# Optimization experiments

Measured on AMD Instinct MI355X. Metric: run time of the kernel, lower is better.

Reference implementation:

```python
import jax, jax.numpy as jnp
import numpy as np

B = 64            # batch size (number of segments)
PTS = 4096        # points per segment
N = B * PTS       # total points
OBS = 128
ACT = 5
HID = 256
LAT = 64
CTX = 128
TEMP = 1.0
LOG2PIE = float(np.log(2.0 * np.pi * np.e))


def _p(key, shape, scale=0.02):
    return (scale * jax.random.normal(key, shape)).astype(jnp.float32)


def setup_inputs() -> dict:
    key = jax.random.key(0)
    ks = jax.random.split(key, 20)
    inp = {
        'obs': jax.random.normal(ks[0], (N, OBS), dtype=jnp.float32),
        'action': jax.random.normal(ks[1], (B, ACT), dtype=jnp.float32),
        'coh_scalar': jax.random.normal(ks[2], (B, 1), dtype=jnp.float32),
        'coh_spatial': jax.random.normal(ks[3], (N,), dtype=jnp.float32),
        'h_prev': jnp.zeros((B, HID), jnp.float32),
        'z_prev': jnp.zeros((B, LAT), jnp.float32),
        'batch': jnp.repeat(jnp.arange(B, dtype=jnp.int64), PTS),
    }
    xin = LAT + ACT + 1  # GRU input: [z_prev, action, coh_scalar]
    inp['W_ih'] = _p(ks[4], (3 * HID, xin)); inp['b_ih'] = jnp.zeros((3 * HID,), jnp.float32)
    inp['W_hh'] = _p(ks[5], (3 * HID, HID)); inp['b_hh'] = jnp.zeros((3 * HID,), jnp.float32)
    inp['W_prior'] = _p(ks[6], (2 * LAT, HID)); inp['b_prior'] = jnp.zeros((2 * LAT,), jnp.float32)
    inp['W_post'] = _p(ks[7], (2 * LAT, HID + OBS)); inp['b_post'] = jnp.zeros((2 * LAT,), jnp.float32)
    inp['W_ae1'] = _p(ks[8], (256, OBS)); inp['b_ae1'] = jnp.zeros((256,), jnp.float32)
    inp['W_ae2'] = _p(ks[9], (OBS, 256)); inp['b_ae2'] = jnp.zeros((OBS,), jnp.float32)
    inp['W_c1'] = _p(ks[10], (512, HID + LAT + OBS)); inp['b_c1'] = jnp.zeros((512,), jnp.float32)
    inp['W_c2'] = _p(ks[11], (CTX, 512)); inp['b_c2'] = jnp.zeros((CTX,), jnp.float32)
    return inp


def _forward(obs, action, coh_scalar, coh_spatial, h_prev, z_prev, batch,
             W_ih, b_ih, W_hh, b_hh, W_prior, b_prior, W_post, b_post,
             W_ae1, b_ae1, W_ae2, b_ae2, W_c1, b_c1, W_c2, b_c2):
    # --- segment mean of obs (the hot scatter-reduce) ---
    counts = jax.ops.segment_sum(jnp.ones((N,), obs.dtype), batch, num_segments=B)
    obs_sum = jax.ops.segment_sum(obs, batch, num_segments=B)            # (B, OBS)
    obs_agg = obs_sum / jnp.maximum(counts, 1.0)[:, None]

    # --- RSSM: GRU cell over [z_prev, action, coh_scalar] ---
    x = jnp.concatenate([z_prev, action, coh_scalar], axis=-1)           # (B, LAT+ACT+1)
    gi = x @ W_ih.T + b_ih
    gh = h_prev @ W_hh.T + b_hh
    gi_r, gi_z, gi_n = jnp.split(gi, 3, axis=-1)
    gh_r, gh_z, gh_n = jnp.split(gh, 3, axis=-1)
    r = jax.nn.sigmoid(gi_r + gh_r)
    u = jax.nn.sigmoid(gi_z + gh_z)
    n = jnp.tanh(gi_n + r * gh_n)
    h = (1.0 - u) * n + u * h_prev                                       # (B, HID)

    prior = h @ W_prior.T + b_prior
    mu_p, logvar_p = jnp.split(prior, 2, axis=-1)
    post = jnp.concatenate([h, obs_agg], axis=-1) @ W_post.T + b_post
    mu_q, logvar_q = jnp.split(post, 2, axis=-1)
    z = mu_q                                                             # deterministic baseline (B, LAT)

    # --- priority: entropy-based uncertainty, per-segment softmax ---
    uncertainty = 0.5 * jnp.sum(logvar_q + LOG2PIE, axis=-1)             # (B,)
    priority = coh_spatial * uncertainty[batch]                          # (N,)
    s = priority / TEMP
    m = jax.ops.segment_max(s, batch, num_segments=B)
    e = jnp.exp(s - m[batch])
    denom = jax.ops.segment_sum(e, batch, num_segments=B)
    priority_norm = e / jnp.maximum(denom, 1e-12)[batch]                 # (N,)

    # --- attended aggregation (second scatter-reduce) ---
    obs_attended = jax.ops.segment_sum(obs * priority_norm[:, None], batch, num_segments=B)  # (B, OBS)
    obs_enc = jax.nn.relu(obs_attended @ W_ae1.T + b_ae1) @ W_ae2.T + b_ae2                  # (B, OBS)

    ctx_in = jnp.concatenate([h, z, obs_enc], axis=-1)                   # (B, HID+LAT+OBS)
    context = jax.nn.relu(ctx_in @ W_c1.T + b_c1) @ W_c2.T + b_c2        # (B, CTX)
    return h, z, context, priority, priority_norm, uncertainty


def reference(obs, action, coh_scalar, coh_spatial, h_prev, z_prev, batch,
              W_ih, b_ih, W_hh, b_hh, W_prior, b_prior, W_post, b_post,
              W_ae1, b_ae1, W_ae2, b_ae2, W_c1, b_c1, W_c2, b_c2):
    return _forward(obs, action, coh_scalar, coh_spatial, h_prev, z_prev, batch,
                    W_ih, b_ih, W_hh, b_hh, W_prior, b_prior, W_post, b_post,
                    W_ae1, b_ae1, W_ae2, b_ae2, W_c1, b_c1, W_c2, b_c2)
```

## Files before the change

kernel.cpp:

```cpp
#include <hip/hip_runtime.h>
#include <math.h>

#define BB   64
#define PTS  4096
#define NTOT (BB * PTS)
#define OBS  128
#define ACT  5
#define HID  256
#define LAT  64
#define CTX  128
#define LOG2PIE 2.8378770664093453f

#define OFF_H   0
#define OFF_Z   (BB * HID)
#define OFF_CTX (OFF_Z + BB * LAT)
#define OFF_PRI (OFF_CTX + BB * CTX)
#define OFF_PN  (OFF_PRI + NTOT)
#define OFF_UNC (OFF_PN + NTOT)

#define CHUNKS 32
#define RPC    (PTS / CHUNKS)

__device__ __forceinline__ float wsum(float v) {
    #pragma unroll
    for (int off = 32; off > 0; off >>= 1) v += __shfl_xor(v, off, 64);
    return v;
}
__device__ __forceinline__ float wmax(float v) {
    #pragma unroll
    for (int off = 32; off > 0; off >>= 1) v = fmaxf(v, __shfl_xor(v, off, 64));
    return v;
}
__device__ __forceinline__ float sigmoidf_(float x) { return 1.f / (1.f + expf(-x)); }

__global__ __launch_bounds__(256) void phase1_kernel(
        const float* __restrict__ obs, float* __restrict__ part,
        const float* __restrict__ action, const float* __restrict__ coh_scalar,
        const float* __restrict__ h_prev, const float* __restrict__ z_prev,
        const float* __restrict__ W_ih, const float* __restrict__ b_ih,
        const float* __restrict__ W_hh, const float* __restrict__ b_hh,
        float* __restrict__ out) {
    __shared__ float4 lds[256];
    int t = threadIdx.x;
    if (blockIdx.x < BB * CHUNKS) {
        int blk = blockIdx.x;
        int b = blk >> 5, chunk = blk & 31;
        int c4 = t & 31, rg = t >> 5;
        const float4* obs4 = (const float4*)obs;
        size_t row0 = (size_t)b * PTS + (size_t)chunk * RPC;
        float4 acc = make_float4(0.f, 0.f, 0.f, 0.f);
        #pragma unroll
        for (int i = 0; i < RPC / 8; ++i) {
            float4 v = obs4[(row0 + rg + 8 * i) * (OBS / 4) + c4];
            acc.x += v.x; acc.y += v.y; acc.z += v.z; acc.w += v.w;
        }
        lds[t] = acc;
        __syncthreads();
        if (t < 32) {
            float4 s = lds[t];
            #pragma unroll
            for (int k = 1; k < 8; ++k) {
                float4 v = lds[t + 32 * k];
                s.x += v.x; s.y += v.y; s.z += v.z; s.w += v.w;
            }
            ((float4*)part)[(size_t)blk * 32 + t] = s;
        }
    } else {
        int wid = (blockIdx.x - BB * CHUNKS) * 4 + (t >> 6);
        int lane = t & 63;
        int b = wid >> 8, j = wid & 255;

        float x0 = z_prev[b * LAT + lane];
        float x1 = 0.f;
        if (lane < ACT) x1 = action[b * ACT + lane];
        else if (lane == ACT) x1 = coh_scalar[b];
        float hp0 = h_prev[b * HID + lane];
        float hp1 = h_prev[b * HID + lane + 64];
        float hp2 = h_prev[b * HID + lane + 128];
        float hp3 = h_prev[b * HID + lane + 192];

        const float* wir = W_ih + (size_t)j * 70;
        const float* wiz = W_ih + (size_t)(HID + j) * 70;
        const float* win = W_ih + (size_t)(2 * HID + j) * 70;
        const float* whr = W_hh + (size_t)j * HID;
        const float* whz = W_hh + (size_t)(HID + j) * HID;
        const float* whn = W_hh + (size_t)(2 * HID + j) * HID;

        float sr = wir[lane] * x0;
        float sz = wiz[lane] * x0;
        float sn = win[lane] * x0;
        if (lane < 6) {
            sr = fmaf(wir[lane + 64], x1, sr);
            sz = fmaf(wiz[lane + 64], x1, sz);
            sn = fmaf(win[lane + 64], x1, sn);
        }
        sr = fmaf(whr[lane], hp0, sr); sr = fmaf(whr[lane + 64], hp1, sr);
        sr = fmaf(whr[lane + 128], hp2, sr); sr = fmaf(whr[lane + 192], hp3, sr);
        sz = fmaf(whz[lane], hp0, sz); sz = fmaf(whz[lane + 64], hp1, sz);
        sz = fmaf(whz[lane + 128], hp2, sz); sz = fmaf(whz[lane + 192], hp3, sz);
        float sh = whn[lane] * hp0;
        sh = fmaf(whn[lane + 64], hp1, sh);
        sh = fmaf(whn[lane + 128], hp2, sh);
        sh = fmaf(whn[lane + 192], hp3, sh);

        sr = wsum(sr); sz = wsum(sz); sn = wsum(sn); sh = wsum(sh);
        if (lane == 0) {
            float r = sigmoidf_(sr + b_ih[j] + b_hh[j]);
            float u = sigmoidf_(sz + b_ih[HID + j] + b_hh[HID + j]);
            float n = tanhf(sn + b_ih[2 * HID + j] + r * (sh + b_hh[2 * HID + j]));
            float h = (1.f - u) * n + u * h_prev[b * HID + j];
            out[OFF_H + b * HID + j] = h;
        }
    }
}

__global__ __launch_bounds__(1024) void post_softmax_kernel(
        const float* __restrict__ part,
        const float* __restrict__ W_post, const float* __restrict__ b_post,
        const float* __restrict__ coh_spatial, float* __restrict__ out) {
    int b = blockIdx.x, t = threadIdx.x;
    int w = t >> 6, lane = t & 63;
    __shared__ __align__(16) float sv[4096];
    __shared__ float hs[256];
    __shared__ float aggs[128];
    __shared__ float lvs[64];
    __shared__ float red[16];
    __shared__ float uS;

    {
        float4* r4 = (float4*)sv;
        int c4 = t & 31, cg = t >> 5;
        const float4* ap4 = (const float4*)part;
        r4[t] = ap4[((size_t)(b * CHUNKS + cg)) * 32 + c4];
    }
    if (t < 256) hs[t] = out[OFF_H + b * HID + t];
    __syncthreads();
    {
        float4* r4 = (float4*)sv;
        #pragma unroll
        for (int s = 16; s > 0; s >>= 1) {
            if ((t >> 5) < s) {
                float4 v = r4[t + 32 * s];
                r4[t].x += v.x; r4[t].y += v.y; r4[t].z += v.z; r4[t].w += v.w;
            }
            __syncthreads();
        }
        if (t < 32) {
            float4 v = r4[t];
            const float sc = 1.0f / PTS;
            aggs[4 * t]     = v.x * sc; aggs[4 * t + 1] = v.y * sc;
            aggs[4 * t + 2] = v.z * sc; aggs[4 * t + 3] = v.w * sc;
        }
    }
    __syncthreads();

    {
        float x0 = hs[lane], x1 = hs[lane + 64], x2 = hs[lane + 128], x3 = hs[lane + 192];
        float x4 = aggs[lane], x5 = aggs[lane + 64];
        #pragma unroll
        for (int g = 0; g < 2; ++g) {
            int r0 = w * 8 + g * 4;
            const float* w0 = W_post + (size_t)r0 * 384;
            const float* w1 = w0 + 384;
            const float* w2 = w0 + 768;
            const float* w3 = w0 + 1152;
            float a0 = w0[lane] * x0, a1 = w1[lane] * x0, a2 = w2[lane] * x0, a3 = w3[lane] * x0;
            a0 = fmaf(w0[lane + 64],  x1, a0); a1 = fmaf(w1[lane + 64],  x1, a1);
            a2 = fmaf(w2[lane + 64],  x1, a2); a3 = fmaf(w3[lane + 64],  x1, a3);
            a0 = fmaf(w0[lane + 128], x2, a0); a1 = fmaf(w1[lane + 128], x2, a1);
            a2 = fmaf(w2[lane + 128], x2, a2); a3 = fmaf(w3[lane + 128], x2, a3);
            a0 = fmaf(w0[lane + 192], x3, a0); a1 = fmaf(w1[lane + 192], x3, a1);
            a2 = fmaf(w2[lane + 192], x3, a2); a3 = fmaf(w3[lane + 192], x3, a3);
            a0 = fmaf(w0[lane + 256], x4, a0); a1 = fmaf(w1[lane + 256], x4, a1);
            a2 = fmaf(w2[lane + 256], x4, a2); a3 = fmaf(w3[lane + 256], x4, a3);
            a0 = fmaf(w0[lane + 320], x5, a0); a1 = fmaf(w1[lane + 320], x5, a1);
            a2 = fmaf(w2[lane + 320], x5, a2); a3 = fmaf(w3[lane + 320], x5, a3);
            a0 = wsum(a0); a1 = wsum(a1); a2 = wsum(a2); a3 = wsum(a3);
            if (lane == 0) {
                a0 += b_post[r0];     a1 += b_post[r0 + 1];
                a2 += b_post[r0 + 2]; a3 += b_post[r0 + 3];
                if (r0 < LAT) {
                    float* dst = out + OFF_Z + b * LAT + r0;
                    dst[0] = a0; dst[1] = a1; dst[2] = a2; dst[3] = a3;
                } else {
                    float* dst = lvs + (r0 - LAT);
                    dst[0] = a0; dst[1] = a1; dst[2] = a2; dst[3] = a3;
                }
            }
        }
    }
    __syncthreads();

    if (w == 0) {
        float v = lvs[lane];
        v = wsum(v);
        if (lane == 0) {
            float u = 0.5f * v + 32.0f * LOG2PIE;
            uS = u;
            out[OFF_UNC + b] = u;
        }
    }
    __syncthreads();
    float u = uS;

    int base = b * PTS;
    float lmax = -INFINITY;
    #pragma unroll
    for (int i = t; i < PTS; i += 1024) {
        float s = coh_spatial[base + i] * u;
        sv[i] = s;
        out[OFF_PRI + base + i] = s;
        lmax = fmaxf(lmax, s);
    }
    lmax = wmax(lmax);
    if (lane == 0) red[w] = lmax;
    __syncthreads();
    float m = red[0];
    #pragma unroll
    for (int k = 1; k < 16; ++k) m = fmaxf(m, red[k]);
    __syncthreads();
    float lsum = 0.f;
    #pragma unroll
    for (int i = t; i < PTS; i += 1024) {
        float e = expf(sv[i] - m);
        sv[i] = e;
        lsum += e;
    }
    lsum = wsum(lsum);
    if (lane == 0) red[w] = lsum;
    __syncthreads();
    float d = 0.f;
    #pragma unroll
    for (int k = 0; k < 16; ++k) d += red[k];
    float inv = 1.f / fmaxf(d, 1e-12f);
    #pragma unroll
    for (int i = t; i < PTS; i += 1024) {
        out[OFF_PN + base + i] = sv[i] * inv;
    }
}

__global__ __launch_bounds__(256) void attn_part_kernel(
        const float* __restrict__ obs, const float* __restrict__ pn,
        float* __restrict__ att_part) {
    int blk = blockIdx.x;
    int b = blk >> 5, chunk = blk & 31;
    int t = threadIdx.x, c4 = t & 31, rg = t >> 5;
    const float4* obs4 = (const float4*)obs;
    size_t row0 = (size_t)b * PTS + (size_t)chunk * RPC;
    float4 acc = make_float4(0.f, 0.f, 0.f, 0.f);
    #pragma unroll
    for (int i = 0; i < RPC / 8; ++i) {
        size_t r = row0 + rg + 8 * i;
        float wgt = pn[r];
        float4 v = obs4[r * (OBS / 4) + c4];
        acc.x = fmaf(v.x, wgt, acc.x);
        acc.y = fmaf(v.y, wgt, acc.y);
        acc.z = fmaf(v.z, wgt, acc.z);
        acc.w = fmaf(v.w, wgt, acc.w);
    }
    __shared__ float4 lds[256];
    lds[t] = acc;
    __syncthreads();
    if (t < 32) {
        float4 s = lds[t];
        #pragma unroll
        for (int k = 1; k < 8; ++k) {
            float4 v = lds[t + 32 * k];
            s.x += v.x; s.y += v.y; s.z += v.z; s.w += v.w;
        }
        ((float4*)att_part)[(size_t)blk * 32 + t] = s;
    }
}

__global__ __launch_bounds__(1024) void head_kernel(
        const float* __restrict__ att_part,
        const float* __restrict__ W_ae1, const float* __restrict__ b_ae1,
        const float* __restrict__ W_ae2, const float* __restrict__ b_ae2,
        const float* __restrict__ W_c1,  const float* __restrict__ b_c1,
        const float* __restrict__ W_c2,  const float* __restrict__ b_c2,
        float* __restrict__ out) {
    int b = blockIdx.x, t = threadIdx.x;
    int w = t >> 6, lane = t & 63;
    __shared__ float4 red4[1024];
    __shared__ float att[128];
    __shared__ float h1[256];
    __shared__ float ctxin[448];
    __shared__ float c1v[512];

    {
        int c4 = t & 31, chunk = t >> 5;
        const float4* ap4 = (const float4*)att_part;
        red4[t] = ap4[((size_t)(b * CHUNKS + chunk)) * 32 + c4];
    }
    if (t < 256) ctxin[t] = out[OFF_H + b * HID + t];
    else if (t < 320) ctxin[t] = out[OFF_Z + b * LAT + (t - 256)];
    __syncthreads();
    #pragma unroll
    for (int s = 16; s > 0; s >>= 1) {
        if ((t >> 5) < s) {
            float4 v = red4[t + 32 * s];
            red4[t].x += v.x; red4[t].y += v.y; red4[t].z += v.z; red4[t].w += v.w;
        }
        __syncthreads();
    }
    if (t < 32) {
        float4 v = red4[t];
        att[4 * t] = v.x; att[4 * t + 1] = v.y; att[4 * t + 2] = v.z; att[4 * t + 3] = v.w;
    }
    __syncthreads();

    {
        float x0 = att[lane], x1 = att[lane + 64];
        #pragma unroll
        for (int g = 0; g < 4; ++g) {
            int r0 = w * 16 + g * 4;
            const float* w0 = W_ae1 + (size_t)(r0 + 0) * OBS;
            const float* w1 = W_ae1 + (size_t)(r0 + 1) * OBS;
            const float* w2 = W_ae1 + (size_t)(r0 + 2) * OBS;
            const float* w3 = W_ae1 + (size_t)(r0 + 3) * OBS;
            float a0 = fmaf(w0[lane + 64], x1, w0[lane] * x0);
            float a1 = fmaf(w1[lane + 64], x1, w1[lane] * x0);
            float a2 = fmaf(w2[lane + 64], x1, w2[lane] * x0);
            float a3 = fmaf(w3[lane + 64], x1, w3[lane] * x0);
            a0 = wsum(a0); a1 = wsum(a1); a2 = wsum(a2); a3 = wsum(a3);
            if (lane == 0) {
                h1[r0]     = fmaxf(a0 + b_ae1[r0],     0.f);
                h1[r0 + 1] = fmaxf(a1 + b_ae1[r0 + 1], 0.f);
                h1[r0 + 2] = fmaxf(a2 + b_ae1[r0 + 2], 0.f);
                h1[r0 + 3] = fmaxf(a3 + b_ae1[r0 + 3], 0.f);
            }
        }
    }
    __syncthreads();

    {
        float x0 = h1[lane], x1 = h1[lane + 64], x2 = h1[lane + 128], x3 = h1[lane + 192];
        #pragma unroll
        for (int g = 0; g < 2; ++g) {
            int r0 = w * 8 + g * 4;
            const float* w0 = W_ae2 + (size_t)(r0 + 0) * 256;
            const float* w1 = W_ae2 + (size_t)(r0 + 1) * 256;
            const float* w2 = W_ae2 + (size_t)(r0 + 2) * 256;
            const float* w3 = W_ae2 + (size_t)(r0 + 3) * 256;
            float a0 = w0[lane] * x0, a1 = w1[lane] * x0, a2 = w2[lane] * x0, a3 = w3[lane] * x0;
            a0 = fmaf(w0[lane + 64], x1, a0);  a1 = fmaf(w1[lane + 64], x1, a1);
            a2 = fmaf(w2[lane + 64], x1, a2);  a3 = fmaf(w3[lane + 64], x1, a3);
            a0 = fmaf(w0[lane + 128], x2, a0); a1 = fmaf(w1[lane + 128], x2, a1);
            a2 = fmaf(w2[lane + 128], x2, a2); a3 = fmaf(w3[lane + 128], x2, a3);
            a0 = fmaf(w0[lane + 192], x3, a0); a1 = fmaf(w1[lane + 192], x3, a1);
            a2 = fmaf(w2[lane + 192], x3, a2); a3 = fmaf(w3[lane + 192], x3, a3);
            a0 = wsum(a0); a1 = wsum(a1); a2 = wsum(a2); a3 = wsum(a3);
            if (lane == 0) {
                ctxin[320 + r0]     = a0 + b_ae2[r0];
                ctxin[320 + r0 + 1] = a1 + b_ae2[r0 + 1];
                ctxin[320 + r0 + 2] = a2 + b_ae2[r0 + 2];
                ctxin[320 + r0 + 3] = a3 + b_ae2[r0 + 3];
            }
        }
    }
    __syncthreads();

    {
        float x0 = ctxin[lane],       x1 = ctxin[lane + 64],  x2 = ctxin[lane + 128];
        float x3 = ctxin[lane + 192], x4 = ctxin[lane + 256], x5 = ctxin[lane + 320];
        float x6 = ctxin[lane + 384];
        #pragma unroll
        for (int g = 0; g < 8; ++g) {
            int r0 = w * 32 + g * 4;
            const float* w0 = W_c1 + (size_t)(r0 + 0) * 448;
            const float* w1 = W_c1 + (size_t)(r0 + 1) * 448;
            const float* w2 = W_c1 + (size_t)(r0 + 2) * 448;
            const float* w3 = W_c1 + (size_t)(r0 + 3) * 448;
            float a0 = w0[lane] * x0, a1 = w1[lane] * x0, a2 = w2[lane] * x0, a3 = w3[lane] * x0;
            a0 = fmaf(w0[lane + 64], x1, a0);  a1 = fmaf(w1[lane + 64], x1, a1);
            a2 = fmaf(w2[lane + 64], x1, a2);  a3 = fmaf(w3[lane + 64], x1, a3);
            a0 = fmaf(w0[lane + 128], x2, a0); a1 = fmaf(w1[lane + 128], x2, a1);
            a2 = fmaf(w2[lane + 128], x2, a2); a3 = fmaf(w3[lane + 128], x2, a3);
            a0 = fmaf(w0[lane + 192], x3, a0); a1 = fmaf(w1[lane + 192], x3, a1);
            a2 = fmaf(w2[lane + 192], x3, a2); a3 = fmaf(w3[lane + 192], x3, a3);
            a0 = fmaf(w0[lane + 256], x4, a0); a1 = fmaf(w1[lane + 256], x4, a1);
            a2 = fmaf(w2[lane + 256], x4, a2); a3 = fmaf(w3[lane + 256], x4, a3);
            a0 = fmaf(w0[lane + 320], x5, a0); a1 = fmaf(w1[lane + 320], x5, a1);
            a2 = fmaf(w2[lane + 320], x5, a2); a3 = fmaf(w3[lane + 320], x5, a3);
            a0 = fmaf(w0[lane + 384], x6, a0); a1 = fmaf(w1[lane + 384], x6, a1);
            a2 = fmaf(w2[lane + 384], x6, a2); a3 = fmaf(w3[lane + 384], x6, a3);
            a0 = wsum(a0); a1 = wsum(a1); a2 = wsum(a2); a3 = wsum(a3);
            if (lane == 0) {
                c1v[r0]     = fmaxf(a0 + b_c1[r0],     0.f);
                c1v[r0 + 1] = fmaxf(a1 + b_c1[r0 + 1], 0.f);
                c1v[r0 + 2] = fmaxf(a2 + b_c1[r0 + 2], 0.f);
                c1v[r0 + 3] = fmaxf(a3 + b_c1[r0 + 3], 0.f);
            }
        }
    }
    __syncthreads();

    {
        float x0 = c1v[lane],       x1 = c1v[lane + 64],  x2 = c1v[lane + 128], x3 = c1v[lane + 192];
        float x4 = c1v[lane + 256], x5 = c1v[lane + 320], x6 = c1v[lane + 384], x7 = c1v[lane + 448];
        #pragma unroll
        for (int g = 0; g < 2; ++g) {
            int r0 = w * 8 + g * 4;
            const float* w0 = W_c2 + (size_t)(r0 + 0) * 512;
            const float* w1 = W_c2 + (size_t)(r0 + 1) * 512;
            const float* w2 = W_c2 + (size_t)(r0 + 2) * 512;
            const float* w3 = W_c2 + (size_t)(r0 + 3) * 512;
            float a0 = w0[lane] * x0, a1 = w1[lane] * x0, a2 = w2[lane] * x0, a3 = w3[lane] * x0;
            a0 = fmaf(w0[lane + 64], x1, a0);  a1 = fmaf(w1[lane + 64], x1, a1);
            a2 = fmaf(w2[lane + 64], x1, a2);  a3 = fmaf(w3[lane + 64], x1, a3);
            a0 = fmaf(w0[lane + 128], x2, a0); a1 = fmaf(w1[lane + 128], x2, a1);
            a2 = fmaf(w2[lane + 128], x2, a2); a3 = fmaf(w3[lane + 128], x2, a3);
            a0 = fmaf(w0[lane + 192], x3, a0); a1 = fmaf(w1[lane + 192], x3, a1);
            a2 = fmaf(w2[lane + 192], x3, a2); a3 = fmaf(w3[lane + 192], x3, a3);
            a0 = fmaf(w0[lane + 256], x4, a0); a1 = fmaf(w1[lane + 256], x4, a1);
            a2 = fmaf(w2[lane + 256], x4, a2); a3 = fmaf(w3[lane + 256], x4, a3);
            a0 = fmaf(w0[lane + 320], x5, a0); a1 = fmaf(w1[lane + 320], x5, a1);
            a2 = fmaf(w2[lane + 320], x5, a2); a3 = fmaf(w3[lane + 320], x5, a3);
            a0 = fmaf(w0[lane + 384], x6, a0); a1 = fmaf(w1[lane + 384], x6, a1);
            a2 = fmaf(w2[lane + 384], x6, a2); a3 = fmaf(w3[lane + 384], x6, a3);
            a0 = fmaf(w0[lane + 448], x7, a0); a1 = fmaf(w1[lane + 448], x7, a1);
            a2 = fmaf(w2[lane + 448], x7, a2); a3 = fmaf(w3[lane + 448], x7, a3);
            a0 = wsum(a0); a1 = wsum(a1); a2 = wsum(a2); a3 = wsum(a3);
            if (lane == 0) {
                float* dst = out + OFF_CTX + b * CTX;
                dst[r0]     = a0 + b_c2[r0];
                dst[r0 + 1] = a1 + b_c2[r0 + 1];
                dst[r0 + 2] = a2 + b_c2[r0 + 2];
                dst[r0 + 3] = a3 + b_c2[r0 + 3];
            }
        }
    }
}

extern "C" void kernel_launch(void* const* d_in, const int* in_sizes, int n_in,
                              void* d_out, int out_size, void* d_ws, size_t ws_size,
                              hipStream_t stream) {
    const float* obs         = (const float*)d_in[0];
    const float* action      = (const float*)d_in[1];
    const float* coh_scalar  = (const float*)d_in[2];
    const float* coh_spatial = (const float*)d_in[3];
    const float* h_prev      = (const float*)d_in[4];
    const float* z_prev      = (const float*)d_in[5];
    const float* W_ih   = (const float*)d_in[7];
    const float* b_ih   = (const float*)d_in[8];
    const float* W_hh   = (const float*)d_in[9];
    const float* b_hh   = (const float*)d_in[10];
    const float* W_post = (const float*)d_in[13];
    const float* b_post = (const float*)d_in[14];
    const float* W_ae1  = (const float*)d_in[15];
    const float* b_ae1  = (const float*)d_in[16];
    const float* W_ae2  = (const float*)d_in[17];
    const float* b_ae2  = (const float*)d_in[18];
    const float* W_c1   = (const float*)d_in[19];
    const float* b_c1   = (const float*)d_in[20];
    const float* W_c2   = (const float*)d_in[21];
    const float* b_c2   = (const float*)d_in[22];

    float* out = (float*)d_out;
    float* part     = (float*)d_ws;
    float* att_part = part + BB * CHUNKS * OBS;

    phase1_kernel<<<BB * CHUNKS + BB * HID / 4, 256, 0, stream>>>(
        obs, part, action, coh_scalar, h_prev, z_prev, W_ih, b_ih, W_hh, b_hh, out);
    post_softmax_kernel<<<BB, 1024, 0, stream>>>(part, W_post, b_post, coh_spatial, out);
    attn_part_kernel<<<BB * CHUNKS, 256, 0, stream>>>(obs, out + OFF_PN, att_part);
    head_kernel<<<BB, 1024, 0, stream>>>(att_part, W_ae1, b_ae1, W_ae2, b_ae2,
                                         W_c1, b_c1, W_c2, b_c2, out);
}
```

Before: 293.8 us.

## Fuse softmax, attention reduce and head into one last-block-finishes kernel

Replaces three tail kernels with one grid of B*CHUNKS blocks. Each block redundantly computes the posterior logvar, uncertainty and the full per-segment softmax statistics, then does its own chunk of the attention-weighted obs reduction. Partials are accumulated with atomics, and the last block per segment, found via a counter, runs the MLP head. This removes two launches and the round trip of priority_norm through global memory, but repeats the W_post GEMV and the softmax 32 times per segment and serialises the head on one block per segment.

```diff
diff --git a/kernel.cpp b/kernel.cpp
--- a/kernel.cpp
+++ b/kernel.cpp
@@ -33,16 +33,44 @@
 }
 __device__ __forceinline__ float sigmoidf_(float x) { return 1.f / (1.f + expf(-x)); }
 
+template <int K>
+__device__ __forceinline__ void rows4_dot(const float* __restrict__ W, int r0,
+                                          const float* __restrict__ x,
+                                          float& a0, float& a1, float& a2, float& a3) {
+    const int lane = threadIdx.x & 63;
+    const float* w0 = W + (size_t)r0 * K;
+    const float* w1 = w0 + K;
+    const float* w2 = w0 + 2 * K;
+    const float* w3 = w0 + 3 * K;
+    float xs = x[lane];
+    a0 = w0[lane] * xs; a1 = w1[lane] * xs; a2 = w2[lane] * xs; a3 = w3[lane] * xs;
+    #pragma unroll
+    for (int s = 1; s < K / 64; ++s) {
+        xs = x[lane + 64 * s];
+        a0 = fmaf(w0[lane + 64 * s], xs, a0);
+        a1 = fmaf(w1[lane + 64 * s], xs, a1);
+        a2 = fmaf(w2[lane + 64 * s], xs, a2);
+        a3 = fmaf(w3[lane + 64 * s], xs, a3);
+    }
+    a0 = wsum(a0); a1 = wsum(a1); a2 = wsum(a2); a3 = wsum(a3);
+}
+
 __global__ __launch_bounds__(256) void phase1_kernel(
         const float* __restrict__ obs, float* __restrict__ part,
         const float* __restrict__ action, const float* __restrict__ coh_scalar,
         const float* __restrict__ h_prev, const float* __restrict__ z_prev,
         const float* __restrict__ W_ih, const float* __restrict__ b_ih,
         const float* __restrict__ W_hh, const float* __restrict__ b_hh,
+        float* __restrict__ att_acc, int* __restrict__ cnt,
         float* __restrict__ out) {
     __shared__ float4 lds[256];
     int t = threadIdx.x;
     if (blockIdx.x < BB * CHUNKS) {
+        if (blockIdx.x == 0) {
+            #pragma unroll
+            for (int i = 0; i < (BB * OBS) / 256; ++i) att_acc[t + 256 * i] = 0.f;
+            if (t < BB) cnt[t] = 0;
+        }
         int blk = blockIdx.x;
         int b = blk >> 5, chunk = blk & 31;
         int c4 = t & 31, rg = t >> 5;
@@ -114,215 +142,174 @@
     }
 }
 
-__global__ __launch_bounds__(1024) void post_softmax_kernel(
-        const float* __restrict__ part,
+__global__ __launch_bounds__(256) void fused_tail_kernel(
+        const float* __restrict__ obs, const float* __restrict__ part,
+        const float* __restrict__ coh_spatial,
         const float* __restrict__ W_post, const float* __restrict__ b_post,
-        const float* __restrict__ coh_spatial, float* __restrict__ out) {
-    int b = blockIdx.x, t = threadIdx.x;
-    int w = t >> 6, lane = t & 63;
-    __shared__ __align__(16) float sv[4096];
-    __shared__ float hs[256];
-    __shared__ float aggs[128];
-    __shared__ float lvs[64];
-    __shared__ float red[16];
-    __shared__ float uS;
-
-    {
-        float4* r4 = (float4*)sv;
-        int c4 = t & 31, cg = t >> 5;
-        const float4* ap4 = (const float4*)part;
-        r4[t] = ap4[((size_t)(b * CHUNKS + cg)) * 32 + c4];
-    }
-    if (t < 256) hs[t] = out[OFF_H + b * HID + t];
-    __syncthreads();
-    {
-        float4* r4 = (float4*)sv;
-        #pragma unroll
-        for (int s = 16; s > 0; s >>= 1) {
-            if ((t >> 5) < s) {
-                float4 v = r4[t + 32 * s];
-                r4[t].x += v.x; r4[t].y += v.y; r4[t].z += v.z; r4[t].w += v.w;
-            }
-            __syncthreads();
-        }
-        if (t < 32) {
-            float4 v = r4[t];
-            const float sc = 1.0f / PTS;
-            aggs[4 * t]     = v.x * sc; aggs[4 * t + 1] = v.y * sc;
-            aggs[4 * t + 2] = v.z * sc; aggs[4 * t + 3] = v.w * sc;
-        }
-    }
-    __syncthreads();
-
-    {
-        float x0 = hs[lane], x1 = hs[lane + 64], x2 = hs[lane + 128], x3 = hs[lane + 192];
-        float x4 = aggs[lane], x5 = aggs[lane + 64];
-        #pragma unroll
-        for (int g = 0; g < 2; ++g) {
-            int r0 = w * 8 + g * 4;
-            const float* w0 = W_post + (size_t)r0 * 384;
-            const float* w1 = w0 + 384;
-            const float* w2 = w0 + 768;
-            const float* w3 = w0 + 1152;
-            float a0 = w0[lane] * x0, a1 = w1[lane] * x0, a2 = w2[lane] * x0, a3 = w3[lane] * x0;
-            a0 = fmaf(w0[lane + 64],  x1, a0); a1 = fmaf(w1[lane + 64],  x1, a1);
-            a2 = fmaf(w2[lane + 64],  x1, a2); a3 = fmaf(w3[lane + 64],  x1, a3);
-            a0 = fmaf(w0[lane + 128], x2, a0); a1 = fmaf(w1[lane + 128], x2, a1);
-            a2 = fmaf(w2[lane + 128], x2, a2); a3 = fmaf(w3[lane + 128], x2, a3);
-            a0 = fmaf(w0[lane + 192], x3, a0); a1 = fmaf(w1[lane + 192], x3, a1);
-            a2 = fmaf(w2[lane + 192], x3, a2); a3 = fmaf(w3[lane + 192], x3, a3);
-            a0 = fmaf(w0[lane + 256], x4, a0); a1 = fmaf(w1[lane + 256], x4, a1);
-            a2 = fmaf(w2[lane + 256], x4, a2); a3 = fmaf(w3[lane + 256], x4, a3);
-            a0 = fmaf(w0[lane + 320], x5, a0); a1 = fmaf(w1[lane + 320], x5, a1);
-            a2 = fmaf(w2[lane + 320], x5, a2); a3 = fmaf(w3[lane + 320], x5, a3);
-            a0 = wsum(a0); a1 = wsum(a1); a2 = wsum(a2); a3 = wsum(a3);
-            if (lane == 0) {
-                a0 += b_post[r0];     a1 += b_post[r0 + 1];
-                a2 += b_post[r0 + 2]; a3 += b_post[r0 + 3];
-                if (r0 < LAT) {
-                    float* dst = out + OFF_Z + b * LAT + r0;
-                    dst[0] = a0; dst[1] = a1; dst[2] = a2; dst[3] = a3;
-                } else {
-                    float* dst = lvs + (r0 - LAT);
-                    dst[0] = a0; dst[1] = a1; dst[2] = a2; dst[3] = a3;
-                }
-            }
-        }
-    }
-    __syncthreads();
-
-    if (w == 0) {
-        float v = lvs[lane];
-        v = wsum(v);
-        if (lane == 0) {
-            float u = 0.5f * v + 32.0f * LOG2PIE;
-            uS = u;
-            out[OFF_UNC + b] = u;
-        }
-    }
-    __syncthreads();
-    float u = uS;
-
-    int base = b * PTS;
-    float lmax = -INFINITY;
-    #pragma unroll
-    for (int i = t; i < PTS; i += 1024) {
-        float s = coh_spatial[base + i] * u;
-        sv[i] = s;
-        out[OFF_PRI + base + i] = s;
-        lmax = fmaxf(lmax, s);
-    }
-    lmax = wmax(lmax);
-    if (lane == 0) red[w] = lmax;
-    __syncthreads();
-    float m = red[0];
-    #pragma unroll
-    for (int k = 1; k < 16; ++k) m = fmaxf(m, red[k]);
-    __syncthreads();
-    float lsum = 0.f;
-    #pragma unroll
-    for (int i = t; i < PTS; i += 1024) {
-        float e = expf(sv[i] - m);
-        sv[i] = e;
-        lsum += e;
-    }
-    lsum = wsum(lsum);
-    if (lane == 0) red[w] = lsum;
-    __syncthreads();
-    float d = 0.f;
-    #pragma unroll
-    for (int k = 0; k < 16; ++k) d += red[k];
-    float inv = 1.f / fmaxf(d, 1e-12f);
-    #pragma unroll
-    for (int i = t; i < PTS; i += 1024) {
-        out[OFF_PN + base + i] = sv[i] * inv;
-    }
-}
-
-__global__ __launch_bounds__(256) void attn_part_kernel(
-        const float* __restrict__ obs, const float* __restrict__ pn,
-        float* __restrict__ att_part) {
-    int blk = blockIdx.x;
-    int b = blk >> 5, chunk = blk & 31;
-    int t = threadIdx.x, c4 = t & 31, rg = t >> 5;
-    const float4* obs4 = (const float4*)obs;
-    size_t row0 = (size_t)b * PTS + (size_t)chunk * RPC;
-    float4 acc = make_float4(0.f, 0.f, 0.f, 0.f);
-    #pragma unroll
-    for (int i = 0; i < RPC / 8; ++i) {
-        size_t r = row0 + rg + 8 * i;
-        float wgt = pn[r];
-        float4 v = obs4[r * (OBS / 4) + c4];
-        acc.x = fmaf(v.x, wgt, acc.x);
-        acc.y = fmaf(v.y, wgt, acc.y);
-        acc.z = fmaf(v.z, wgt, acc.z);
-        acc.w = fmaf(v.w, wgt, acc.w);
-    }
-    __shared__ float4 lds[256];
-    lds[t] = acc;
-    __syncthreads();
-    if (t < 32) {
-        float4 s = lds[t];
-        #pragma unroll
-        for (int k = 1; k < 8; ++k) {
-            float4 v = lds[t + 32 * k];
-            s.x += v.x; s.y += v.y; s.z += v.z; s.w += v.w;
-        }
-        ((float4*)att_part)[(size_t)blk * 32 + t] = s;
-    }
-}
-
-__global__ __launch_bounds__(1024) void head_kernel(
-        const float* __restrict__ att_part,
         const float* __restrict__ W_ae1, const float* __restrict__ b_ae1,
         const float* __restrict__ W_ae2, const float* __restrict__ b_ae2,
         const float* __restrict__ W_c1,  const float* __restrict__ b_c1,
         const float* __restrict__ W_c2,  const float* __restrict__ b_c2,
+        float* __restrict__ att_acc, int* __restrict__ cnt,
         float* __restrict__ out) {
-    int b = blockIdx.x, t = threadIdx.x;
-    int w = t >> 6, lane = t & 63;
-    __shared__ float4 red4[1024];
-    __shared__ float att[128];
+    const int blk = blockIdx.x, b = blk >> 5, chunk = blk & 31;
+    const int t = threadIdx.x, w = t >> 6, lane = t & 63;
+
+    __shared__ float hsagg[384];
+    __shared__ float ss[4096];
+    __shared__ float lvs[64];
+    __shared__ float red[4];
+    __shared__ float4 red4[256];
+    __shared__ float uS;
+    __shared__ int lastS;
+    __shared__ float attS[128];
+    __shared__ float ctxin[448];
     __shared__ float h1[256];
-    __shared__ float ctxin[448];
     __shared__ float c1v[512];
 
-    {
-        int c4 = t & 31, chunk = t >> 5;
-        const float4* ap4 = (const float4*)att_part;
-        red4[t] = ap4[((size_t)(b * CHUNKS + chunk)) * 32 + c4];
-    }
-    if (t < 256) ctxin[t] = out[OFF_H + b * HID + t];
-    else if (t < 320) ctxin[t] = out[OFF_Z + b * LAT + (t - 256)];
-    __syncthreads();
-    #pragma unroll
-    for (int s = 16; s > 0; s >>= 1) {
-        if ((t >> 5) < s) {
-            float4 v = red4[t + 32 * s];
-            red4[t].x += v.x; red4[t].y += v.y; red4[t].z += v.z; red4[t].w += v.w;
-        }
+    hsagg[t] = out[OFF_H + b * HID + t];
+    {
+        const int c = t & 127, half = t >> 7;
+        const float* p = part + (size_t)b * (CHUNKS * OBS) + (size_t)half * 16 * OBS + c;
+        float s = 0.f;
+        #pragma unroll
+        for (int k = 0; k < 16; ++k) s += p[k * OBS];
+        ss[t] = s;
+    }
+    __syncthreads();
+    if (t < 128) hsagg[256 + t] = (ss[t] + ss[t + 128]) * (1.0f / PTS);
+    __syncthreads();
+
+    {
+        float a0, a1, a2, a3;
+        #pragma unroll
+        for (int g = 0; g < 4; ++g) {
+            int r0 = 64 + w * 16 + g * 4;
+            rows4_dot<384>(W_post, r0, hsagg, a0, a1, a2, a3);
+            if (lane == 0) {
+                lvs[r0 - 64] = a0 + b_post[r0];
+                lvs[r0 - 63] = a1 + b_post[r0 + 1];
+                lvs[r0 - 62] = a2 + b_post[r0 + 2];
+                lvs[r0 - 61] = a3 + b_post[r0 + 3];
+            }
+        }
+        if (chunk == 0) {
+            #pragma unroll
+            for (int g = 0; g < 4; ++g) {
+                int r0 = w * 16 + g * 4;
+                rows4_dot<384>(W_post, r0, hsagg, a0, a1, a2, a3);
+                if (lane == 0) {
+                    float* dst = out + OFF_Z + b * LAT + r0;
+                    dst[0] = a0 + b_post[r0];     dst[1] = a1 + b_post[r0 + 1];
+                    dst[2] = a2 + b_post[r0 + 2]; dst[3] = a3 + b_post[r0 + 3];
+                }
+            }
+        }
+    }
+    __syncthreads();
+    if (w == 0) {
+        float v = wsum(lvs[lane]);
+        if (lane == 0) {
+            float uu = 0.5f * v + 32.0f * LOG2PIE;
+            uS = uu;
+            if (chunk == 0) out[OFF_UNC + b] = uu;
+        }
+    }
+    __syncthreads();
+    const float u = uS;
+
+    const int base = b * PTS;
+    float lmax = -INFINITY;
+    #pragma unroll
+    for (int k = 0; k < 16; ++k) {
+        int i = t + 256 * k;
+        float s = coh_spatial[base + i] * u;
+        ss[i] = s;
+        lmax = fmaxf(lmax, s);
+    }
+    lmax = wmax(lmax);
+    if (lane == 0) red[w] = lmax;
+    __syncthreads();
+    const float m = fmaxf(fmaxf(red[0], red[1]), fmaxf(red[2], red[3]));
+    if (t < 128) out[OFF_PRI + base + chunk * RPC + t] = ss[chunk * RPC + t];
+    __syncthreads();
+    float lsum = 0.f;
+    #pragma unroll
+    for (int k = 0; k < 16; ++k) {
+        int i = t + 256 * k;
+        float e = expf(ss[i] - m);
+        ss[i] = e;
+        lsum += e;
+    }
+    lsum = wsum(lsum);
+    if (lane == 0) red[w] = lsum;
+    __syncthreads();
+    const float inv = 1.0f / fmaxf(red[0] + red[1] + red[2] + red[3], 1e-12f);
+    if (t < 128) out[OFF_PN + base + chunk * RPC + t] = ss[chunk * RPC + t] * inv;
+
+    {
+        const int c4 = t & 31, rg = t >> 5;
+        const float4* obs4 = (const float4*)obs;
+        const size_t row0 = (size_t)b * PTS + (size_t)chunk * RPC;
+        float4 acc = make_float4(0.f, 0.f, 0.f, 0.f);
+        #pragma unroll
+        for (int i2 = 0; i2 < RPC / 8; ++i2) {
+            int r = rg + 8 * i2;
+            float wgt = ss[chunk * RPC + r] * inv;
+            float4 v = obs4[(row0 + r) * (OBS / 4) + c4];
+            acc.x = fmaf(v.x, wgt, acc.x);
+            acc.y = fmaf(v.y, wgt, acc.y);
+            acc.z = fmaf(v.z, wgt, acc.z);
+            acc.w = fmaf(v.w, wgt, acc.w);
+        }
+        red4[t] = acc;
         __syncthreads();
-    }
-    if (t < 32) {
-        float4 v = red4[t];
-        att[4 * t] = v.x; att[4 * t + 1] = v.y; att[4 * t + 2] = v.z; att[4 * t + 3] = v.w;
-    }
-    __syncthreads();
-
-    {
-        float x0 = att[lane], x1 = att[lane + 64];
+        if (t < 32) {
+            float4 s4 = red4[t];
+            #pragma unroll
+            for (int k = 1; k < 8; ++k) {
+                float4 v = red4[t + 32 * k];
+                s4.x += v.x; s4.y += v.y; s4.z += v.z; s4.w += v.w;
+            }
+            float* dst = att_acc + b * OBS + 4 * t;
+            atomicAdd(dst + 0, s4.x); atomicAdd(dst + 1, s4.y);
+            atomicAdd(dst + 2, s4.z); atomicAdd(dst + 3, s4.w);
+        }
+    }
+    __syncthreads();
+    if (t == 0) {
+        __threadfence();
+        int old = atomicAdd(&cnt[b], 1);
+        lastS = (old == CHUNKS - 1) ? 1 : 0;
+    }
+    __syncthreads();
+    if (!lastS) return;
+    __threadfence();
+
+    if (t < 128)
+        attS[t] = __hip_atomic_load(&att_acc[b * OBS + t], __ATOMIC_ACQUIRE,
+                                    __HIP_MEMORY_SCOPE_AGENT);
+    ctxin[t] = hsagg[t];
+    {
+        float a0, a1, a2, a3;
         #pragma unroll
         for (int g = 0; g < 4; ++g) {
             int r0 = w * 16 + g * 4;
-            const float* w0 = W_ae1 + (size_t)(r0 + 0) * OBS;
-            const float* w1 = W_ae1 + (size_t)(r0 + 1) * OBS;
-            const float* w2 = W_ae1 + (size_t)(r0 + 2) * OBS;
-            const float* w3 = W_ae1 + (size_t)(r0 + 3) * OBS;
-            float a0 = fmaf(w0[lane + 64], x1, w0[lane] * x0);
-            float a1 = fmaf(w1[lane + 64], x1, w1[lane] * x0);
-            float a2 = fmaf(w2[lane + 64], x1, w2[lane] * x0);
-            float a3 = fmaf(w3[lane + 64], x1, w3[lane] * x0);
-            a0 = wsum(a0); a1 = wsum(a1); a2 = wsum(a2); a3 = wsum(a3);
+            rows4_dot<384>(W_post, r0, hsagg, a0, a1, a2, a3);
+            if (lane == 0) {
+                ctxin[256 + r0]     = a0 + b_post[r0];
+                ctxin[256 + r0 + 1] = a1 + b_post[r0 + 1];
+                ctxin[256 + r0 + 2] = a2 + b_post[r0 + 2];
+                ctxin[256 + r0 + 3] = a3 + b_post[r0 + 3];
+            }
+        }
+    }
+    __syncthreads();
+    {
+        float a0, a1, a2, a3;
+        for (int g = 0; g < 16; ++g) {
+            int r0 = w * 64 + g * 4;
+            rows4_dot<128>(W_ae1, r0, attS, a0, a1, a2, a3);
             if (lane == 0) {
                 h1[r0]     = fmaxf(a0 + b_ae1[r0],     0.f);
                 h1[r0 + 1] = fmaxf(a1 + b_ae1[r0 + 1], 0.f);
@@ -332,24 +319,11 @@
         }
     }
     __syncthreads();
-
-    {
-        float x0 = h1[lane], x1 = h1[lane + 64], x2 = h1[lane + 128], x3 = h1[lane + 192];
-        #pragma unroll
-        for (int g = 0; g < 2; ++g) {
-            int r0 = w * 8 + g * 4;
-            const float* w0 = W_ae2 + (size_t)(r0 + 0) * 256;
-            const float* w1 = W_ae2 + (size_t)(r0 + 1) * 256;
-            const float* w2 = W_ae2 + (size_t)(r0 + 2) * 256;
-            const float* w3 = W_ae2 + (size_t)(r0 + 3) * 256;
-            float a0 = w0[lane] * x0, a1 = w1[lane] * x0, a2 = w2[lane] * x0, a3 = w3[lane] * x0;
-            a0 = fmaf(w0[lane + 64], x1, a0);  a1 = fmaf(w1[lane + 64], x1, a1);
-            a2 = fmaf(w2[lane + 64], x1, a2);  a3 = fmaf(w3[lane + 64], x1, a3);
-            a0 = fmaf(w0[lane + 128], x2, a0); a1 = fmaf(w1[lane + 128], x2, a1);
-            a2 = fmaf(w2[lane + 128], x2, a2); a3 = fmaf(w3[lane + 128], x2, a3);
-            a0 = fmaf(w0[lane + 192], x3, a0); a1 = fmaf(w1[lane + 192], x3, a1);
-            a2 = fmaf(w2[lane + 192], x3, a2); a3 = fmaf(w3[lane + 192], x3, a3);
-            a0 = wsum(a0); a1 = wsum(a1); a2 = wsum(a2); a3 = wsum(a3);
+    {
+        float a0, a1, a2, a3;
+        for (int g = 0; g < 8; ++g) {
+            int r0 = w * 32 + g * 4;
+            rows4_dot<256>(W_ae2, r0, h1, a0, a1, a2, a3);
             if (lane == 0) {
                 ctxin[320 + r0]     = a0 + b_ae2[r0];
                 ctxin[320 + r0 + 1] = a1 + b_ae2[r0 + 1];
@@ -359,32 +333,11 @@
         }
     }
     __syncthreads();
-
-    {
-        float x0 = ctxin[lane],       x1 = ctxin[lane + 64],  x2 = ctxin[lane + 128];
-        float x3 = ctxin[lane + 192], x4 = ctxin[lane + 256], x5 = ctxin[lane + 320];
-        float x6 = ctxin[lane + 384];
-        #pragma unroll
-        for (int g = 0; g < 8; ++g) {
-            int r0 = w * 32 + g * 4;
-            const float* w0 = W_c1 + (size_t)(r0 + 0) * 448;
-            const float* w1 = W_c1 + (size_t)(r0 + 1) * 448;
-            const float* w2 = W_c1 + (size_t)(r0 + 2) * 448;
-            const float* w3 = W_c1 + (size_t)(r0 + 3) * 448;
-            float a0 = w0[lane] * x0, a1 = w1[lane] * x0, a2 = w2[lane] * x0, a3 = w3[lane] * x0;
-            a0 = fmaf(w0[lane + 64], x1, a0);  a1 = fmaf(w1[lane + 64], x1, a1);
-            a2 = fmaf(w2[lane + 64], x1, a2);  a3 = fmaf(w3[lane + 64], x1, a3);
-            a0 = fmaf(w0[lane + 128], x2, a0); a1 = fmaf(w1[lane + 128], x2, a1);
-            a2 = fmaf(w2[lane + 128], x2, a2); a3 = fmaf(w3[lane + 128], x2, a3);
-            a0 = fmaf(w0[lane + 192], x3, a0); a1 = fmaf(w1[lane + 192], x3, a1);
-            a2 = fmaf(w2[lane + 192], x3, a2); a3 = fmaf(w3[lane + 192], x3, a3);
-            a0 = fmaf(w0[lane + 256], x4, a0); a1 = fmaf(w1[lane + 256], x4, a1);
-            a2 = fmaf(w2[lane + 256], x4, a2); a3 = fmaf(w3[lane + 256], x4, a3);
-            a0 = fmaf(w0[lane + 320], x5, a0); a1 = fmaf(w1[lane + 320], x5, a1);
-            a2 = fmaf(w2[lane + 320], x5, a2); a3 = fmaf(w3[lane + 320], x5, a3);
-            a0 = fmaf(w0[lane + 384], x6, a0); a1 = fmaf(w1[lane + 384], x6, a1);
-            a2 = fmaf(w2[lane + 384], x6, a2); a3 = fmaf(w3[lane + 384], x6, a3);
-            a0 = wsum(a0); a1 = wsum(a1); a2 = wsum(a2); a3 = wsum(a3);
+    {
+        float a0, a1, a2, a3;
+        for (int g = 0; g < 32; ++g) {
+            int r0 = w * 128 + g * 4;
+            rows4_dot<448>(W_c1, r0, ctxin, a0, a1, a2, a3);
             if (lane == 0) {
                 c1v[r0]     = fmaxf(a0 + b_c1[r0],     0.f);
                 c1v[r0 + 1] = fmaxf(a1 + b_c1[r0 + 1], 0.f);
@@ -394,39 +347,15 @@
         }
     }
     __syncthreads();
-
-    {
-        float x0 = c1v[lane],       x1 = c1v[lane + 64],  x2 = c1v[lane + 128], x3 = c1v[lane + 192];
-        float x4 = c1v[lane + 256], x5 = c1v[lane + 320], x6 = c1v[lane + 384], x7 = c1v[lane + 448];
-        #pragma unroll
-        for (int g = 0; g < 2; ++g) {
-            int r0 = w * 8 + g * 4;
-            const float* w0 = W_c2 + (size_t)(r0 + 0) * 512;
-            const float* w1 = W_c2 + (size_t)(r0 + 1) * 512;
-            const float* w2 = W_c2 + (size_t)(r0 + 2) * 512;
-            const float* w3 = W_c2 + (size_t)(r0 + 3) * 512;
-            float a0 = w0[lane] * x0, a1 = w1[lane] * x0, a2 = w2[lane] * x0, a3 = w3[lane] * x0;
-            a0 = fmaf(w0[lane + 64], x1, a0);  a1 = fmaf(w1[lane + 64], x1, a1);
-            a2 = fmaf(w2[lane + 64], x1, a2);  a3 = fmaf(w3[lane + 64], x1, a3);
-            a0 = fmaf(w0[lane + 128], x2, a0); a1 = fmaf(w1[lane + 128], x2, a1);
-            a2 = fmaf(w2[lane + 128], x2, a2); a3 = fmaf(w3[lane + 128], x2, a3);
-            a0 = fmaf(w0[lane + 192], x3, a0); a1 = fmaf(w1[lane + 192], x3, a1);
-            a2 = fmaf(w2[lane + 192], x3, a2); a3 = fmaf(w3[lane + 192], x3, a3);
-            a0 = fmaf(w0[lane + 256], x4, a0); a1 = fmaf(w1[lane + 256], x4, a1);
-            a2 = fmaf(w2[lane + 256], x4, a2); a3 = fmaf(w3[lane + 256], x4, a3);
-            a0 = fmaf(w0[lane + 320], x5, a0); a1 = fmaf(w1[lane + 320], x5, a1);
-            a2 = fmaf(w2[lane + 320], x5, a2); a3 = fmaf(w3[lane + 320], x5, a3);
-            a0 = fmaf(w0[lane + 384], x6, a0); a1 = fmaf(w1[lane + 384], x6, a1);
-            a2 = fmaf(w2[lane + 384], x6, a2); a3 = fmaf(w3[lane + 384], x6, a3);
-            a0 = fmaf(w0[lane + 448], x7, a0); a1 = fmaf(w1[lane + 448], x7, a1);
-            a2 = fmaf(w2[lane + 448], x7, a2); a3 = fmaf(w3[lane + 448], x7, a3);
-            a0 = wsum(a0); a1 = wsum(a1); a2 = wsum(a2); a3 = wsum(a3);
-            if (lane == 0) {
-                float* dst = out + OFF_CTX + b * CTX;
-                dst[r0]     = a0 + b_c2[r0];
-                dst[r0 + 1] = a1 + b_c2[r0 + 1];
-                dst[r0 + 2] = a2 + b_c2[r0 + 2];
-                dst[r0 + 3] = a3 + b_c2[r0 + 3];
+    {
+        float a0, a1, a2, a3;
+        for (int g = 0; g < 8; ++g) {
+            int r0 = w * 32 + g * 4;
+            rows4_dot<512>(W_c2, r0, c1v, a0, a1, a2, a3);
+            if (lane == 0) {
+                float* dst = out + OFF_CTX + b * CTX + r0;
+                dst[0] = a0 + b_c2[r0];     dst[1] = a1 + b_c2[r0 + 1];
+                dst[2] = a2 + b_c2[r0 + 2]; dst[3] = a3 + b_c2[r0 + 3];
             }
         }
     }
@@ -456,14 +385,15 @@
     const float* W_c2   = (const float*)d_in[21];
     const float* b_c2   = (const float*)d_in[22];
 
-    float* out = (float*)d_out;
+    float* out      = (float*)d_out;
     float* part     = (float*)d_ws;
-    float* att_part = part + BB * CHUNKS * OBS;
+    float* att_acc  = part + BB * CHUNKS * OBS;
+    int*   cnt      = (int*)(att_acc + BB * OBS);
 
     phase1_kernel<<<BB * CHUNKS + BB * HID / 4, 256, 0, stream>>>(
-        obs, part, action, coh_scalar, h_prev, z_prev, W_ih, b_ih, W_hh, b_hh, out);
-    post_softmax_kernel<<<BB, 1024, 0, stream>>>(part, W_post, b_post, coh_spatial, out);
-    attn_part_kernel<<<BB * CHUNKS, 256, 0, stream>>>(obs, out + OFF_PN, att_part);
-    head_kernel<<<BB, 1024, 0, stream>>>(att_part, W_ae1, b_ae1, W_ae2, b_ae2,
-                                         W_c1, b_c1, W_c2, b_c2, out);
-}
+        obs, part, action, coh_scalar, h_prev, z_prev, W_ih, b_ih, W_hh, b_hh,
+        att_acc, cnt, out);
+    fused_tail_kernel<<<BB * CHUNKS, 256, 0, stream>>>(
+        obs, part, coh_spatial, W_post, b_post, W_ae1, b_ae1, W_ae2, b_ae2,
+        W_c1, b_c1, W_c2, b_c2, att_acc, cnt, out);
+}
```

Result: slower. 542.2 us (+84.5%).
